# Kernel tuning notes

Hardware: AMD Instinct MI355X
Metric: run time of the kernel (lower is better)

The kernel has to match this reference:

```python
import jax, jax.numpy as jnp
import numpy as np

NUM_EMBEDDINGS = 1024
EMBEDDING_DIM = 64
BETA = 0.25


def setup_inputs() -> dict:
    key = jax.random.key(0)
    k1, k2 = jax.random.split(key)
    inputs = jax.random.normal(k1, (16, 64, 64, 64), dtype=jnp.float32)
    # tf.random_uniform_initializer default: uniform in [-0.05, 0.05]
    embedding = jax.random.uniform(k2, (NUM_EMBEDDINGS, EMBEDDING_DIM),
                                   dtype=jnp.float32, minval=-0.05, maxval=0.05)
    return {"inputs": inputs, "embedding": embedding}


def reference(inputs, embedding):
    input_shape = inputs.shape
    flat = inputs.reshape(-1, EMBEDDING_DIM)  # [N, D]
    # squared L2 distances to each codebook entry: [N, K]
    distances = (jnp.sum(flat * flat, axis=1, keepdims=True)
                 + jnp.sum(embedding * embedding, axis=1)
                 - 2.0 * jnp.einsum('nd,kd->nk', flat, embedding))
    idx = jnp.argmin(distances, axis=1)  # [N]
    # one-hot @ embedding is just a gather of codebook rows
    quantized = embedding[idx].reshape(input_shape)

    # Keras MSE reduces over the last axis (per-element losses), then
    # add_loss aggregates; we take the mean to get the scalar VQ loss.
    commitment_loss = jnp.mean(jnp.mean(
        (jax.lax.stop_gradient(quantized) - inputs) ** 2, axis=-1))
    codebook_loss = jnp.mean(jnp.mean(
        (quantized - jax.lax.stop_gradient(inputs)) ** 2, axis=-1))
    loss = codebook_loss + BETA * commitment_loss

    # straight-through estimator
    quantized_ste = inputs + jax.lax.stop_gradient(quantized - inputs)
    return quantized_ste, loss
```

## Files before the change

### kernel.cpp

```cpp
#include <hip/hip_runtime.h>
#include <math.h>

#define NROWS 65536
#define D     64
#define K     1024
#define NCT   8
#define BR    128
#define BC    128
#define BETA  0.25f
#define SCALE 1024.0f
#define THR   200.0f

typedef _Float16 half8  __attribute__((ext_vector_type(8)));
typedef float    f32x4  __attribute__((ext_vector_type(4)));
typedef unsigned long long u64;

#define WS_BP   0u
#define WS_EN   (256u*1024)
#define WS_EN2  (260u*1024)
#define WS_FID  (264u*1024)
#define WS_LIST (WS_FID + 256u*1024)
#define WS_CNT  (WS_LIST + 256u*1024)
#define WS_PART (WS_CNT + 256u)

static __device__ __forceinline__ unsigned ordf(float f) {
    unsigned b = __float_as_uint(f);
    return (b & 0x80000000u) ? ~b : (b | 0x80000000u);
}
static __device__ __forceinline__ void gload_lds16(const void* g, void* l) {
    __builtin_amdgcn_global_load_lds(
        (const __attribute__((address_space(1))) unsigned*)g,
        (__attribute__((address_space(3))) unsigned*)l,
        16, 0, 0);
}

__global__ __launch_bounds__(256) void vq_prep(const float* __restrict__ emb,
                                               float* __restrict__ enorm,
                                               float* __restrict__ enorm2,
                                               char* __restrict__ Bp,
                                               unsigned* __restrict__ counter) {
    if (blockIdx.x == 0 && threadIdx.x == 0) counter[0] = 0u;
    int k = blockIdx.x * 256 + threadIdx.x;
    if (k >= K) return;
    const int ct = k >> 7, r = k & 127;
    char* base = Bp + (size_t)ct * 32768 + (size_t)r * 128;
    const float4* e4 = (const float4*)(emb + (size_t)k * D);
    float s = 0.f;
    #pragma unroll
    for (int c = 0; c < 8; ++c) {
        float4 ea = e4[2 * c], eb = e4[2 * c + 1];
        s += ea.x * ea.x + ea.y * ea.y + ea.z * ea.z + ea.w * ea.w;
        s += eb.x * eb.x + eb.y * eb.y + eb.z * eb.z + eb.w * eb.w;
        float sc[8] = {ea.x * SCALE, ea.y * SCALE, ea.z * SCALE, ea.w * SCALE,
                       eb.x * SCALE, eb.y * SCALE, eb.z * SCALE, eb.w * SCALE};
        half8 hh, hl;
        #pragma unroll
        for (int e = 0; e < 8; ++e) {
            _Float16 h = (_Float16)sc[e];
            hh[e] = h;
            hl[e] = (_Float16)(sc[e] - (float)h);
        }
        int off = ((c ^ (r & 7)) << 4);
        *(half8*)(base + off)         = hh;
        *(half8*)(base + 16384 + off) = hl;
    }
    enorm[k]  = s;
    enorm2[k] = s * (SCALE * SCALE);
}

__global__ __launch_bounds__(256, 2) void vq_gemm(const float* __restrict__ x,
                                                  const char* __restrict__ Bp,
                                                  const float* __restrict__ enorm2,
                                                  unsigned* __restrict__ fid,
                                                  unsigned* __restrict__ list,
                                                  unsigned* __restrict__ counter) {
    __shared__ __align__(16) char bufB[2][32768];

    const int tid  = threadIdx.x;
    const int lane = tid & 63, w = tid >> 6;
    const int fr   = lane & 15;
    const int kg   = lane >> 4;
    const int rb   = (int)blockIdx.x * BR;

    const float4* x4 = (const float4*)x;
    half8 ah[2][2], al[2][2];
    #pragma unroll
    for (int fi = 0; fi < 2; ++fi) {
        #pragma unroll
        for (int kk = 0; kk < 2; ++kk) {
            int row = rb + w * 32 + fi * 16 + fr;
            float4 v0 = x4[(size_t)row * 16 + kk * 8 + kg * 2];
            float4 v1 = x4[(size_t)row * 16 + kk * 8 + kg * 2 + 1];
            float sc[8] = {v0.x * SCALE, v0.y * SCALE, v0.z * SCALE, v0.w * SCALE,
                           v1.x * SCALE, v1.y * SCALE, v1.z * SCALE, v1.w * SCALE};
            #pragma unroll
            for (int e = 0; e < 8; ++e) {
                _Float16 h = (_Float16)sc[e];
                ah[fi][kk][e] = h;
                al[fi][kk][e] = (_Float16)(sc[e] - (float)h);
            }
        }
    }

    {
        const char* gsrc = Bp + (size_t)w * 8192 + (size_t)lane * 16;
        char* ldst = &bufB[0][w * 8192];
        #pragma unroll
        for (int j = 0; j < 8; ++j)
            gload_lds16(gsrc + j * 1024, ldst + j * 1024);
    }

    float d1[2][4], d2[2][4];
    int   i1[2][4];
    #pragma unroll
    for (int fi = 0; fi < 2; ++fi)
        #pragma unroll
        for (int rg = 0; rg < 4; ++rg) {
            d1[fi][rg] = 3.4e38f; d2[fi][rg] = 3.4e38f; i1[fi][rg] = 0;
        }

    for (int ct = 0; ct < NCT; ++ct) {
        const int  cb  = ct * BC;
        const int  buf = ct & 1;
        __syncthreads();

        if (ct < NCT - 1) {
            const char* gsrc = Bp + (size_t)(ct + 1) * 32768 + (size_t)w * 8192
                             + (size_t)lane * 16;
            char* ldst = &bufB[buf ^ 1][w * 8192];
            #pragma unroll
            for (int j = 0; j < 8; ++j)
                gload_lds16(gsrc + j * 1024, ldst + j * 1024);
        }

        float en2f[8];
        #pragma unroll
        for (int ci = 0; ci < 8; ++ci)
            en2f[ci] = enorm2[cb + ci * 16 + fr];
        const int idxb = cb + fr;

        const char* bb = &bufB[buf][0];

        #pragma unroll
        for (int g = 0; g < 2; ++g) {
            f32x4 acc[2][4];
            #pragma unroll
            for (int fi = 0; fi < 2; ++fi)
                #pragma unroll
                for (int i = 0; i < 4; ++i) acc[fi][i] = (f32x4){0.f, 0.f, 0.f, 0.f};

            #pragma unroll
            for (int kk = 0; kk < 2; ++kk) {
                const int chunk = ((kk * 4 + kg) ^ (fr & 7)) << 4;
                half8 bf[4];
                #pragma unroll
                for (int i = 0; i < 4; ++i)
                    bf[i] = *(const half8*)(bb + ((g * 4 + i) * 16 + fr) * 128 + chunk);
                #pragma unroll
                for (int fi = 0; fi < 2; ++fi)
                    #pragma unroll
                    for (int i = 0; i < 4; ++i)
                        acc[fi][i] = __builtin_amdgcn_mfma_f32_16x16x32_f16(ah[fi][kk], bf[i], acc[fi][i], 0, 0, 0);
                #pragma unroll
                for (int fi = 0; fi < 2; ++fi)
                    #pragma unroll
                    for (int i = 0; i < 4; ++i)
                        acc[fi][i] = __builtin_amdgcn_mfma_f32_16x16x32_f16(al[fi][kk], bf[i], acc[fi][i], 0, 0, 0);
                #pragma unroll
                for (int i = 0; i < 4; ++i)
                    bf[i] = *(const half8*)(bb + 16384 + ((g * 4 + i) * 16 + fr) * 128 + chunk);
                #pragma unroll
                for (int fi = 0; fi < 2; ++fi)
                    #pragma unroll
                    for (int i = 0; i < 4; ++i)
                        acc[fi][i] = __builtin_amdgcn_mfma_f32_16x16x32_f16(ah[fi][kk], bf[i], acc[fi][i], 0, 0, 0);
            }

            #pragma unroll
            for (int fi = 0; fi < 2; ++fi) {
                #pragma unroll
                for (int rg = 0; rg < 4; ++rg) {
                    #pragma unroll
                    for (int i = 0; i < 4; ++i) {
                        float d  = fmaf(-2.f, acc[fi][i][rg], en2f[g * 4 + i]);
                        int  idx = idxb + (g * 4 + i) * 16;
                        bool lt  = d < d1[fi][rg];
                        d2[fi][rg] = fminf(fmaxf(d1[fi][rg], d), d2[fi][rg]);
                        i1[fi][rg] = lt ? idx : i1[fi][rg];
                        d1[fi][rg] = fminf(d1[fi][rg], d);
                    }
                }
            }
        }
    }

    #pragma unroll
    for (int fi = 0; fi < 2; ++fi) {
        #pragma unroll
        for (int rg = 0; rg < 4; ++rg) {
            float v1 = d1[fi][rg], v2 = d2[fi][rg];
            int   ii = i1[fi][rg];
            #pragma unroll
            for (int off = 8; off >= 1; off >>= 1) {
                float o1 = __shfl_xor(v1, off, 16);
                float o2 = __shfl_xor(v2, off, 16);
                int   oi = __shfl_xor(ii, off, 16);
                float loser = fmaxf(v1, o1);
                v2 = fminf(fminf(v2, o2), loser);
                bool bt = o1 < v1;
                v1 = fminf(v1, o1);
                ii = bt ? oi : ii;
            }
            if (fr == 0) {
                int row = rb + w * 32 + fi * 16 + kg * 4 + rg;
                if (v2 - v1 > THR) {
                    fid[row] = (unsigned)ii;
                } else {
                    unsigned pos = atomicAdd(counter, 1u);
                    list[pos] = (unsigned)row;
                }
            }
        }
    }
}

__global__ __launch_bounds__(256) void vq_fallback(const float* __restrict__ x,
                                                   const float* __restrict__ emb,
                                                   const float* __restrict__ enorm,
                                                   const unsigned* __restrict__ list,
                                                   const unsigned* __restrict__ counter,
                                                   unsigned* __restrict__ final_idx) {
    __shared__ float4 xr[16];
    __shared__ u64 red[256];
    const int tid = threadIdx.x;
    const unsigned total = counter[0];
    for (unsigned i = blockIdx.x; i < total; i += gridDim.x) {
        const int n = (int)list[i];
        __syncthreads();
        if (tid < 16) xr[tid] = ((const float4*)x)[(size_t)n * 16 + tid];
        __syncthreads();
        float xnorm = 0.f;
        #pragma unroll
        for (int q = 0; q < 16; ++q) {
            float4 v = xr[q];
            xnorm += v.x * v.x + v.y * v.y + v.z * v.z + v.w * v.w;
        }
        u64 best = ~0ull;
        #pragma unroll
        for (int j = 0; j < 4; ++j) {
            int k = tid + j * 256;
            const float4* e4 = (const float4*)(emb + (size_t)k * D);
            float d0 = 0.f, d1v = 0.f, d2v = 0.f, d3v = 0.f;
            #pragma unroll
            for (int q = 0; q < 4; ++q) {
                float4 ea = e4[q*4+0], eb = e4[q*4+1], ec = e4[q*4+2], ed = e4[q*4+3];
                float4 va = xr[q*4+0], vb = xr[q*4+1], vc = xr[q*4+2], vd = xr[q*4+3];
                d0  = fmaf(va.w, ea.w, fmaf(va.z, ea.z, fmaf(va.y, ea.y, fmaf(va.x, ea.x, d0))));
                d1v = fmaf(vb.w, eb.w, fmaf(vb.z, eb.z, fmaf(vb.y, eb.y, fmaf(vb.x, eb.x, d1v))));
                d2v = fmaf(vc.w, ec.w, fmaf(vc.z, ec.z, fmaf(vc.y, ec.y, fmaf(vc.x, ec.x, d2v))));
                d3v = fmaf(vd.w, ed.w, fmaf(vd.z, ed.z, fmaf(vd.y, ed.y, fmaf(vd.x, ed.x, d3v))));
            }
            float dot  = (d0 + d1v) + (d2v + d3v);
            float dist = fmaf(-2.f, dot, xnorm + enorm[k]);
            u64 pk = ((u64)ordf(dist) << 32) | (unsigned)k;
            if (pk < best) best = pk;
        }
        red[tid] = best;
        __syncthreads();
        for (int s = 128; s > 0; s >>= 1) {
            if (tid < s) red[tid] = red[tid] < red[tid+s] ? red[tid] : red[tid+s];
            __syncthreads();
        }
        if (tid == 0) final_idx[n] = (unsigned)(red[0] & 0xFFFFFFFFu);
    }
}

__global__ __launch_bounds__(256) void vq_out(const float* __restrict__ x,
                                              const float* __restrict__ emb,
                                              const unsigned* __restrict__ final_idx,
                                              float* __restrict__ out,
                                              float* __restrict__ partial) {
    __shared__ int   lds_idx[256];
    __shared__ float lds_red[256];
    const int tid   = threadIdx.x;
    const int rbase = blockIdx.x * 256;
    const int n     = rbase + tid;

    lds_idx[tid] = (int)(final_idx[n] & 0xFFFFu);
    __syncthreads();

    const float4* x4 = (const float4*)x;
    const float4* e4 = (const float4*)emb;
    float4* o4 = (float4*)out;
    float err = 0.f;
    #pragma unroll
    for (int i = 0; i < 16; ++i) {
        int f = i * 256 + tid;
        int row = f >> 4, col = f & 15;
        int e = lds_idx[row];
        float4 q = e4[(size_t)e * 16 + col];
        float4 v = x4[(size_t)rbase * 16 + f];
        float ax = q.x - v.x, ay = q.y - v.y, az = q.z - v.z, aw = q.w - v.w;
        err += ax * ax + ay * ay + az * az + aw * aw;
        o4[(size_t)rbase * 16 + f] = q;
    }
    __syncthreads();
    lds_red[tid] = err;
    __syncthreads();
    for (int s = 128; s > 0; s >>= 1) {
        if (tid < s) lds_red[tid] += lds_red[tid + s];
        __syncthreads();
    }
    if (tid == 0) partial[blockIdx.x] = lds_red[0];
}

__global__ __launch_bounds__(256) void vq_finish(const float* __restrict__ partial,
                                                 float* __restrict__ loss_out) {
    __shared__ float lds[256];
    int tid = threadIdx.x;
    lds[tid] = partial[tid];
    __syncthreads();
    for (int s = 128; s > 0; s >>= 1) {
        if (tid < s) lds[tid] += lds[tid + s];
        __syncthreads();
    }
    if (tid == 0) loss_out[0] = (1.0f + BETA) * lds[0] / (float)(NROWS * D);
}

extern "C" void kernel_launch(void* const* d_in, const int* in_sizes, int n_in,
                              void* d_out, int out_size, void* d_ws, size_t ws_size,
                              hipStream_t stream) {
    const float* x   = (const float*)d_in[0];
    const float* emb = (const float*)d_in[1];
    float* out = (float*)d_out;
    char* ws = (char*)d_ws;

    char* Bp          = ws + WS_BP;
    float* enorm      = (float*)(ws + WS_EN);
    float* enorm2     = (float*)(ws + WS_EN2);
    unsigned* fid     = (unsigned*)(ws + WS_FID);
    unsigned* list    = (unsigned*)(ws + WS_LIST);
    unsigned* counter = (unsigned*)(ws + WS_CNT);
    float* partial    = (float*)(ws + WS_PART);

    vq_prep<<<K / 256, 256, 0, stream>>>(emb, enorm, enorm2, Bp, counter);
    vq_gemm<<<NROWS / BR, 256, 0, stream>>>(x, Bp, enorm2, fid, list, counter);
    vq_fallback<<<128, 256, 0, stream>>>(x, emb, enorm, list, counter, fid);
    vq_out<<<NROWS / 256, 256, 0, stream>>>(x, emb, fid, out, partial);
    vq_finish<<<1, 256, 0, stream>>>(partial, out + (size_t)NROWS * D);
}
```

Measured before the change: 61.79 us.

## Fuse gather/output and loss accumulation into GEMM and fallback kernels

```diff
diff --git a/kernel.cpp b/kernel.cpp
--- a/kernel.cpp
+++ b/kernel.cpp
@@ -10,6 +10,7 @@
 #define BETA  0.25f
 #define SCALE 1024.0f
 #define THR   200.0f
+#define FXS   1048576.0
 
 typedef _Float16 half8  __attribute__((ext_vector_type(8)));
 typedef float    f32x4  __attribute__((ext_vector_type(4)));
@@ -18,10 +19,9 @@
 #define WS_BP   0u
 #define WS_EN   (256u*1024)
 #define WS_EN2  (260u*1024)
-#define WS_FID  (264u*1024)
-#define WS_LIST (WS_FID + 256u*1024)
+#define WS_LIST (264u*1024)
 #define WS_CNT  (WS_LIST + 256u*1024)
-#define WS_PART (WS_CNT + 256u)
+#define WS_ERR  (WS_CNT + 128u)
 
 static __device__ __forceinline__ unsigned ordf(float f) {
     unsigned b = __float_as_uint(f);
@@ -38,8 +38,9 @@
                                                float* __restrict__ enorm,
                                                float* __restrict__ enorm2,
                                                char* __restrict__ Bp,
-                                               unsigned* __restrict__ counter) {
-    if (blockIdx.x == 0 && threadIdx.x == 0) counter[0] = 0u;
+                                               unsigned* __restrict__ counter,
+                                               u64* __restrict__ errAcc) {
+    if (blockIdx.x == 0 && threadIdx.x == 0) { counter[0] = 0u; errAcc[0] = 0ull; }
     int k = blockIdx.x * 256 + threadIdx.x;
     if (k >= K) return;
     const int ct = k >> 7, r = k & 127;
@@ -70,11 +71,14 @@
 
 __global__ __launch_bounds__(256, 2) void vq_gemm(const float* __restrict__ x,
                                                   const char* __restrict__ Bp,
+                                                  const float* __restrict__ emb,
                                                   const float* __restrict__ enorm2,
-                                                  unsigned* __restrict__ fid,
+                                                  float* __restrict__ out,
                                                   unsigned* __restrict__ list,
-                                                  unsigned* __restrict__ counter) {
+                                                  unsigned* __restrict__ counter,
+                                                  u64* __restrict__ errAcc) {
     __shared__ __align__(16) char bufB[2][32768];
+    __shared__ float redE[256];
 
     const int tid  = threadIdx.x;
     const int lane = tid & 63, w = tid >> 6;
@@ -194,6 +198,9 @@
         }
     }
 
+    const float4* e4g = (const float4*)emb;
+    float4* o4 = (float4*)out;
+    float errp = 0.f;
     #pragma unroll
     for (int fi = 0; fi < 2; ++fi) {
         #pragma unroll
@@ -211,17 +218,29 @@
                 v1 = fminf(v1, o1);
                 ii = bt ? oi : ii;
             }
-            if (fr == 0) {
-                int row = rb + w * 32 + fi * 16 + kg * 4 + rg;
-                if (v2 - v1 > THR) {
-                    fid[row] = (unsigned)ii;
-                } else {
-                    unsigned pos = atomicAdd(counter, 1u);
-                    list[pos] = (unsigned)row;
-                }
-            }
-        }
-    }
+            int row = rb + w * 32 + fi * 16 + kg * 4 + rg;
+            if (v2 - v1 > THR) {
+                float4 q = e4g[(size_t)ii * 16 + fr];
+                float4 v = x4[(size_t)row * 16 + fr];
+                o4[(size_t)row * 16 + fr] = q;
+                float ax = q.x - v.x, ay = q.y - v.y, az = q.z - v.z, aw = q.w - v.w;
+                errp += ax * ax + ay * ay + az * az + aw * aw;
+            } else if (fr == 0) {
+                unsigned pos = atomicAdd(counter, 1u);
+                list[pos] = (unsigned)row;
+            }
+        }
+    }
+
+    __syncthreads();
+    redE[tid] = errp;
+    __syncthreads();
+    for (int s = 128; s > 0; s >>= 1) {
+        if (tid < s) redE[tid] += redE[tid + s];
+        __syncthreads();
+    }
+    if (tid == 0)
+        atomicAdd(errAcc, (u64)((double)redE[0] * FXS + 0.5));
 }
 
 __global__ __launch_bounds__(256) void vq_fallback(const float* __restrict__ x,
@@ -229,11 +248,14 @@
                                                    const float* __restrict__ enorm,
                                                    const unsigned* __restrict__ list,
                                                    const unsigned* __restrict__ counter,
-                                                   unsigned* __restrict__ final_idx) {
+                                                   float* __restrict__ out,
+                                                   u64* __restrict__ errAcc) {
     __shared__ float4 xr[16];
     __shared__ u64 red[256];
+    __shared__ float errv[16];
     const int tid = threadIdx.x;
     const unsigned total = counter[0];
+    u64 qerr = 0ull;
     for (unsigned i = blockIdx.x; i < total; i += gridDim.x) {
         const int n = (int)list[i];
         __syncthreads();
@@ -271,60 +293,31 @@
             if (tid < s) red[tid] = red[tid] < red[tid+s] ? red[tid] : red[tid+s];
             __syncthreads();
         }
-        if (tid == 0) final_idx[n] = (unsigned)(red[0] & 0xFFFFFFFFu);
-    }
-}
-
-__global__ __launch_bounds__(256) void vq_out(const float* __restrict__ x,
-                                              const float* __restrict__ emb,
-                                              const unsigned* __restrict__ final_idx,
-                                              float* __restrict__ out,
-                                              float* __restrict__ partial) {
-    __shared__ int   lds_idx[256];
-    __shared__ float lds_red[256];
-    const int tid   = threadIdx.x;
-    const int rbase = blockIdx.x * 256;
-    const int n     = rbase + tid;
-
-    lds_idx[tid] = (int)(final_idx[n] & 0xFFFFu);
-    __syncthreads();
-
-    const float4* x4 = (const float4*)x;
-    const float4* e4 = (const float4*)emb;
-    float4* o4 = (float4*)out;
-    float err = 0.f;
-    #pragma unroll
-    for (int i = 0; i < 16; ++i) {
-        int f = i * 256 + tid;
-        int row = f >> 4, col = f & 15;
-        int e = lds_idx[row];
-        float4 q = e4[(size_t)e * 16 + col];
-        float4 v = x4[(size_t)rbase * 16 + f];
-        float ax = q.x - v.x, ay = q.y - v.y, az = q.z - v.z, aw = q.w - v.w;
-        err += ax * ax + ay * ay + az * az + aw * aw;
-        o4[(size_t)rbase * 16 + f] = q;
-    }
-    __syncthreads();
-    lds_red[tid] = err;
-    __syncthreads();
-    for (int s = 128; s > 0; s >>= 1) {
-        if (tid < s) lds_red[tid] += lds_red[tid + s];
-        __syncthreads();
-    }
-    if (tid == 0) partial[blockIdx.x] = lds_red[0];
-}
-
-__global__ __launch_bounds__(256) void vq_finish(const float* __restrict__ partial,
-                                                 float* __restrict__ loss_out) {
-    __shared__ float lds[256];
-    int tid = threadIdx.x;
-    lds[tid] = partial[tid];
-    __syncthreads();
-    for (int s = 128; s > 0; s >>= 1) {
-        if (tid < s) lds[tid] += lds[tid + s];
-        __syncthreads();
-    }
-    if (tid == 0) loss_out[0] = (1.0f + BETA) * lds[0] / (float)(NROWS * D);
+        const int bi = (int)(red[0] & 0xFFFFFFFFu);
+        if (tid < 16) {
+            float4 q = ((const float4*)emb)[(size_t)bi * 16 + tid];
+            float4 v = xr[tid];
+            ((float4*)out)[(size_t)n * 16 + tid] = q;
+            float ax = q.x - v.x, ay = q.y - v.y, az = q.z - v.z, aw = q.w - v.w;
+            errv[tid] = ax * ax + ay * ay + az * az + aw * aw;
+        }
+        __syncthreads();
+        if (tid == 0) {
+            float re = 0.f;
+            #pragma unroll
+            for (int j = 0; j < 16; ++j) re += errv[j];
+            qerr += (u64)((double)re * FXS + 0.5);
+        }
+    }
+    if (tid == 0 && qerr) atomicAdd(errAcc, qerr);
+}
+
+__global__ __launch_bounds__(64) void vq_finish(const u64* __restrict__ errAcc,
+                                                float* __restrict__ loss_out) {
+    if (threadIdx.x == 0) {
+        double s = (double)errAcc[0] / FXS;
+        loss_out[0] = (float)((1.0 + (double)BETA) * s / (double)((size_t)NROWS * D));
+    }
 }
 
 extern "C" void kernel_launch(void* const* d_in, const int* in_sizes, int n_in,
@@ -338,14 +331,12 @@
     char* Bp          = ws + WS_BP;
     float* enorm      = (float*)(ws + WS_EN);
     float* enorm2     = (float*)(ws + WS_EN2);
-    unsigned* fid     = (unsigned*)(ws + WS_FID);
     unsigned* list    = (unsigned*)(ws + WS_LIST);
     unsigned* counter = (unsigned*)(ws + WS_CNT);
-    float* partial    = (float*)(ws + WS_PART);
-
-    vq_prep<<<K / 256, 256, 0, stream>>>(emb, enorm, enorm2, Bp, counter);
-    vq_gemm<<<NROWS / BR, 256, 0, stream>>>(x, Bp, enorm2, fid, list, counter);
-    vq_fallback<<<128, 256, 0, stream>>>(x, emb, enorm, list, counter, fid);
-    vq_out<<<NROWS / 256, 256, 0, stream>>>(x, emb, fid, out, partial);
-    vq_finish<<<1, 256, 0, stream>>>(partial, out + (size_t)NROWS * D);
-}
+    u64* errAcc       = (u64*)(ws + WS_ERR);
+
+    vq_prep<<<K / 256, 256, 0, stream>>>(emb, enorm, enorm2, Bp, counter, errAcc);
+    vq_gemm<<<NROWS / BR, 256, 0, stream>>>(x, Bp, emb, enorm2, out, list, counter, errAcc);
+    vq_fallback<<<128, 256, 0, stream>>>(x, emb, enorm, list, counter, out, errAcc);
+    vq_finish<<<1, 64, 0, stream>>>(errAcc, out + (size_t)NROWS * D);
+}
```

Result: no change. 61.59 us (-0.3%).
